# Performance work log

Hardware: AMD Instinct MI355X
Metric: run time of the kernel (lower is better)

## Reference

```python
import jax, jax.numpy as jnp
import numpy as np

DIM = 256          # model dim
H = 8              # num heads
E = DIM // H       # head dim = 32
M = 32             # ball size
NB = 8192          # number of balls
N = NB * M         # total points = 262144
D3 = 3             # spatial dimensionality


def setup_inputs() -> dict:
    key = jax.random.key(0)
    ks = jax.random.split(key, 10)
    s = 1.0 / np.sqrt(DIM)
    return {
        "x": jax.random.normal(ks[0], (N, DIM), jnp.float32),
        "pos": jax.random.normal(ks[1], (N, D3), jnp.float32),
        "w_qkv": jax.random.normal(ks[2], (DIM, 3 * DIM), jnp.float32) * s,
        "b_qkv": jnp.zeros((3 * DIM,), jnp.float32),
        "w_pe": jax.random.normal(ks[3], (D3, DIM), jnp.float32) * (1.0 / np.sqrt(D3)),
        "b_pe": jnp.zeros((DIM,), jnp.float32),
        "w_proj": jax.random.normal(ks[4], (DIM, DIM), jnp.float32) * s,
        "b_proj": jnp.zeros((DIM,), jnp.float32),
        "sigma_att": -1.0 + 0.01 * jax.random.normal(ks[5], (1, H, 1, 1), jnp.float32),
    }


def reference(x, pos, w_qkv, b_qkv, w_pe, b_pe, w_proj, b_proj, sigma_att):
    n = x.shape[0] // M
    pos_b = pos.reshape(n, M, D3)                       # (n, m, 3)

    # eq. 9: relative position embedding wrt ball center
    centers = pos_b.mean(axis=1, keepdims=True)         # (n, 1, 3)
    rel = (pos_b - centers).reshape(n * M, D3)
    x = x + rel @ w_pe + b_pe                           # (N, DIM)

    # qkv projection; layout '(H E K)' with K fastest
    qkv = (x @ w_qkv + b_qkv).reshape(n, M, H, E, 3)
    q = jnp.transpose(qkv[..., 0], (0, 2, 1, 3))        # (n, H, m, E)
    k = jnp.transpose(qkv[..., 1], (0, 2, 1, 3))
    v = jnp.transpose(qkv[..., 2], (0, 2, 1, 3))

    # eq. 10: distance-based attention bias
    diff = pos_b[:, :, None, :] - pos_b[:, None, :, :]  # (n, m, m, 3)
    d2 = jnp.sum(diff * diff, axis=-1)
    dist = jnp.sqrt(jnp.maximum(d2, 1e-12))             # safe sqrt (grad at 0)
    bias = sigma_att * dist[:, None, :, :]              # (n, H, m, m)

    scale = 1.0 / np.sqrt(E)
    scores = jnp.einsum('nhme,nhke->nhmk', q, k) * scale + bias
    attn = jax.nn.softmax(scores, axis=-1)
    out = jnp.einsum('nhmk,nhke->nhme', attn, v)        # (n, H, m, E)
    out = jnp.transpose(out, (0, 2, 1, 3)).reshape(n * M, DIM)
    return out @ w_proj + b_proj
```

## Files before the change

kernel.cpp:

```cpp
#include <hip/hip_runtime.h>

#define NPTS   262144
#define NBALLS 8192
#define MSZ    32

typedef unsigned short u16;
typedef __attribute__((ext_vector_type(8))) unsigned short u16x8;
typedef __attribute__((ext_vector_type(4))) unsigned short u16x4;
typedef __attribute__((ext_vector_type(8))) __bf16 bf16x8;
typedef __attribute__((ext_vector_type(4))) float f32x4;

__device__ inline u16 f2bf(float f) {
    unsigned u = __builtin_bit_cast(unsigned, f);
    u += 0x7fffu + ((u >> 16) & 1u);
    return (u16)(u >> 16);
}

__device__ inline f32x4 mfma16(u16x8 a, u16x8 b, f32x4 c) {
    return __builtin_amdgcn_mfma_f32_16x16x32_bf16(
        __builtin_bit_cast(bf16x8, a), __builtin_bit_cast(bf16x8, b), c, 0, 0, 0);
}

__device__ inline void gload_lds16(const u16* g, u16* l) {
    __builtin_amdgcn_global_load_lds(
        (const __attribute__((address_space(1))) void*)g,
        (__attribute__((address_space(3))) void*)l, 16, 0, 0);
}

__global__ __launch_bounds__(256) void k0_wprep(const float* __restrict__ w_qkv,
                                                const float* __restrict__ b_qkv,
                                                const float* __restrict__ w_proj,
                                                u16* __restrict__ wqkvT,
                                                u16* __restrict__ wpF,
                                                float* __restrict__ bq) {
    int idx = blockIdx.x * 256 + threadIdx.x;
    if (idx < 768 * 256) {
        int cp = idx >> 8, r = idx & 255;
        int k = cp >> 8, rem = cp & 255, h = rem >> 5, e = rem & 31;
        int orig = h * 96 + e * 3 + k;
        wqkvT[cp * 256 + r] = f2bf(w_qkv[r * 768 + orig]);
        if (r == 0) bq[cp] = b_qkv[orig];
    } else {
        int tid2 = idx - 768 * 256;
        int lane = tid2 & 63, ch = tid2 >> 6;
        int hk = ch & 7, gct = ch >> 3;
        int r15 = lane & 15, g4 = lane >> 4;
        u16x8 o;
#pragma unroll
        for (int j = 0; j < 8; ++j)
            o[j] = f2bf(w_proj[(size_t)(hk * 32 + g4 * 8 + j) * 256 + gct * 16 + r15]);
        *(u16x8*)&wpF[(size_t)tid2 * 8] = o;
    }
}

__global__ __launch_bounds__(256) void k0b_xp(const float* __restrict__ x,
                                              const float* __restrict__ pos,
                                              const float* __restrict__ w_pe,
                                              const float* __restrict__ b_pe,
                                              u16* __restrict__ xp) {
    int ball = blockIdx.x, t = threadIdx.x;
    __shared__ float ps[MSZ][3];
    __shared__ float ctr[3];
    if (t < MSZ * 3) ((float*)ps)[t] = pos[(size_t)ball * (MSZ * 3) + t];
    __syncthreads();
    if (t < 3) {
        float s = 0.f;
#pragma unroll
        for (int j = 0; j < MSZ; ++j) s += ps[j][t];
        ctr[t] = s * (1.0f / MSZ);
    }
    __syncthreads();
    int c4 = (t & 63) * 4;
    float4 w0 = *(const float4*)&w_pe[c4];
    float4 w1 = *(const float4*)&w_pe[256 + c4];
    float4 w2 = *(const float4*)&w_pe[512 + c4];
    float4 bp = *(const float4*)&b_pe[c4];
#pragma unroll
    for (int mi = (t >> 6); mi < MSZ; mi += 4) {
        float rx = ps[mi][0] - ctr[0], ry = ps[mi][1] - ctr[1], rz = ps[mi][2] - ctr[2];
        size_t row = (size_t)ball * MSZ + mi;
        float4 xv = *(const float4*)&x[row * 256 + c4];
        u16x4 o;
        o.x = f2bf(xv.x + rx * w0.x + ry * w1.x + rz * w2.x + bp.x);
        o.y = f2bf(xv.y + rx * w0.y + ry * w1.y + rz * w2.y + bp.y);
        o.z = f2bf(xv.z + rx * w0.z + ry * w1.z + rz * w2.z + bp.z);
        o.w = f2bf(xv.w + rx * w0.w + ry * w1.w + rz * w2.w + bp.w);
        *(u16x4*)&xp[row * 256 + c4] = o;
    }
}

__global__ __launch_bounds__(512, 4) void k1_qkv(const u16* __restrict__ xp,
                                                 const u16* __restrict__ wqkvT,
                                                 const float* __restrict__ bq,
                                                 u16* __restrict__ qkv2) {
    __shared__ __align__(16) u16 As[2][128 * 64];
    __shared__ __align__(16) u16 Bs[2][128 * 64];
    int id = blockIdx.x;
    int wk = (id >> 3) + (id & 7) * 1536;
    int ct = wk % 6, rt = wk / 6;
    int t = threadIdx.x;
    int lane = t & 63, wv = t >> 6;
    int r15 = lane & 15, g4 = lane >> 4;
    int wr = wv >> 1, wc = wv & 1;
    int rowbase = rt * 128, colbase = ct * 128;

    f32x4 acc[2][4];
#pragma unroll
    for (int i = 0; i < 2; ++i)
#pragma unroll
        for (int j = 0; j < 4; ++j) acc[i][j] = (f32x4){0.f, 0.f, 0.f, 0.f};

#pragma unroll
    for (int i = 0; i < 2; ++i) {
        int c = i * 512 + t;
        int row = c >> 3, sg = c & 7;
        int gsw = (sg ^ (row & 7)) * 8;
        gload_lds16(&xp[(size_t)(rowbase + row) * 256 + gsw], &As[0][c * 8]);
        gload_lds16(&wqkvT[(size_t)(colbase + row) * 256 + gsw], &Bs[0][c * 8]);
    }
    __syncthreads();

    for (int kt = 0; kt < 4; ++kt) {
        int cur = kt & 1;
        if (kt < 3) {
            int k0 = (kt + 1) * 64;
#pragma unroll
            for (int i = 0; i < 2; ++i) {
                int c = i * 512 + t;
                int row = c >> 3, sg = c & 7;
                int gsw = k0 + (sg ^ (row & 7)) * 8;
                gload_lds16(&xp[(size_t)(rowbase + row) * 256 + gsw], &As[cur ^ 1][c * 8]);
                gload_lds16(&wqkvT[(size_t)(colbase + row) * 256 + gsw], &Bs[cur ^ 1][c * 8]);
            }
        }
#pragma unroll
        for (int ks = 0; ks < 2; ++ks) {
            u16x8 a[2], b[4];
#pragma unroll
            for (int i = 0; i < 2; ++i) {
                int R = wr * 32 + i * 16 + r15;
                a[i] = *(const u16x8*)&As[cur][R * 64 + (((ks * 4 + g4) ^ (R & 7)) * 8)];
            }
#pragma unroll
            for (int j = 0; j < 4; ++j) {
                int C = wc * 64 + j * 16 + r15;
                b[j] = *(const u16x8*)&Bs[cur][C * 64 + (((ks * 4 + g4) ^ (C & 7)) * 8)];
            }
#pragma unroll
            for (int i = 0; i < 2; ++i)
#pragma unroll
                for (int j = 0; j < 4; ++j)
                    acc[i][j] = mfma16(a[i], b[j], acc[i][j]);
        }
        __syncthreads();
    }

    const int ball = rt * 4 + wr;
#pragma unroll
    for (int j = 0; j < 4; ++j) {
        int cp = colbase + wc * 64 + j * 16 + r15;
        float bias = bq[cp];
        int mat = cp >> 8, rem = cp & 255, h = rem >> 5, e = rem & 31;
        size_t base = (size_t)ball * 24576 + mat * 8192 + h * 1024 + e;
#pragma unroll
        for (int i = 0; i < 2; ++i) {
#pragma unroll
            for (int r = 0; r < 4; ++r) {
                int point = i * 16 + g4 * 4 + r;
                qkv2[base + point * 32] = f2bf(acc[i][j][r] + bias);
            }
        }
    }
}

__global__ __launch_bounds__(256) void k23_attnproj(const float* __restrict__ pos,
                                                    const float* __restrict__ sigma,
                                                    const u16* __restrict__ qkv2,
                                                    const u16* __restrict__ wpF,
                                                    const float* __restrict__ bp,
                                                    float* __restrict__ out) {
    int ball = blockIdx.x, t = threadIdx.x;
    __shared__ float ps[MSZ][3];
    __shared__ float dist_s[MSZ][33];
    __shared__ __align__(16) u16 V_s[MSZ][256];
    __shared__ __align__(16) u16 P_s[4][MSZ][40];
    __shared__ __align__(16) u16 ao_s[MSZ][264];

    const size_t ballbase = (size_t)ball * 24576;

    if (t < MSZ * 3) ((float*)ps)[t] = pos[(size_t)ball * (MSZ * 3) + t];
    __syncthreads();
    for (int p = t; p < 1024; p += 256) {
        int m = p >> 5, k = p & 31;
        float dx = ps[m][0] - ps[k][0], dy = ps[m][1] - ps[k][1], dz = ps[m][2] - ps[k][2];
        dist_s[m][k] = sqrtf(fmaxf(dx * dx + dy * dy + dz * dz, 1e-12f));
    }
#pragma unroll
    for (int i = 0; i < 4; ++i) {
        int c = i * 256 + t;
        int h = c >> 7, wi = c & 127;
        int point = wi >> 2, g4w = wi & 3;
        int col8 = h * 32 + g4w * 8;
        int cs = col8 ^ (((point >> 3) & 3) << 4);
        *(u16x8*)&V_s[point][cs] = *(const u16x8*)&qkv2[ballbase + 16384 + (size_t)c * 8];
    }
    __syncthreads();

    int lane = t & 63, wv = t >> 6;
    int r15 = lane & 15, g4 = lane >> 4;
    const float scale = 0.17677669529663687f;

#pragma unroll
    for (int hh = 0; hh < 2; ++hh) {
        int h = wv * 2 + hh;
        float sig = sigma[h];
        u16x8 aq[2], bk[2];
#pragma unroll
        for (int i = 0; i < 2; ++i) {
            aq[i] = *(const u16x8*)&qkv2[ballbase + h * 1024 + (size_t)(i * 16 + r15) * 32 + g4 * 8];
            bk[i] = *(const u16x8*)&qkv2[ballbase + 8192 + h * 1024 + (size_t)(i * 16 + r15) * 32 + g4 * 8];
        }
        f32x4 s[2][2];
#pragma unroll
        for (int i = 0; i < 2; ++i)
#pragma unroll
            for (int j = 0; j < 2; ++j) s[i][j] = (f32x4){0.f, 0.f, 0.f, 0.f};
#pragma unroll
        for (int i = 0; i < 2; ++i)
#pragma unroll
            for (int j = 0; j < 2; ++j)
                s[i][j] = mfma16(aq[i], bk[j], s[i][j]);

#pragma unroll
        for (int i = 0; i < 2; ++i) {
#pragma unroll
            for (int r = 0; r < 4; ++r) {
                int row = i * 16 + g4 * 4 + r;
                float v0 = s[i][0][r] * scale + sig * dist_s[row][r15];
                float v1 = s[i][1][r] * scale + sig * dist_s[row][16 + r15];
                float m = fmaxf(v0, v1);
                m = fmaxf(m, __shfl_xor(m, 1));
                m = fmaxf(m, __shfl_xor(m, 2));
                m = fmaxf(m, __shfl_xor(m, 4));
                m = fmaxf(m, __shfl_xor(m, 8));
                float e0 = __expf(v0 - m), e1 = __expf(v1 - m);
                float su = e0 + e1;
                su += __shfl_xor(su, 1);
                su += __shfl_xor(su, 2);
                su += __shfl_xor(su, 4);
                su += __shfl_xor(su, 8);
                float rin = 1.0f / su;
                P_s[wv][row][r15]      = f2bf(e0 * rin);
                P_s[wv][row][16 + r15] = f2bf(e1 * rin);
            }
        }
        u16x8 pa[2];
#pragma unroll
        for (int i = 0; i < 2; ++i)
            pa[i] = *(const u16x8*)&P_s[wv][i * 16 + r15][g4 * 8];
        u16x8 bv[2];
#pragma unroll
        for (int j = 0; j < 2; ++j) {
#pragma unroll
            for (int jj = 0; jj < 8; ++jj) {
                int kp = g4 * 8 + jj;
                int colv = h * 32 + j * 16 + r15;
                bv[j][jj] = V_s[kp][colv ^ (((kp >> 3) & 3) << 4)];
            }
        }
        f32x4 o[2][2];
#pragma unroll
        for (int i = 0; i < 2; ++i)
#pragma unroll
            for (int j = 0; j < 2; ++j) o[i][j] = (f32x4){0.f, 0.f, 0.f, 0.f};
#pragma unroll
        for (int i = 0; i < 2; ++i)
#pragma unroll
            for (int j = 0; j < 2; ++j)
                o[i][j] = mfma16(pa[i], bv[j], o[i][j]);
#pragma unroll
        for (int i = 0; i < 2; ++i)
#pragma unroll
            for (int j = 0; j < 2; ++j)
#pragma unroll
                for (int r = 0; r < 4; ++r) {
                    int row = i * 16 + g4 * 4 + r;
                    int col = h * 32 + j * 16 + r15;
                    ao_s[row][col] = f2bf(o[i][j][r]);
                }
    }
    __syncthreads();

    f32x4 pacc[4][2];
#pragma unroll
    for (int tt = 0; tt < 4; ++tt)
#pragma unroll
        for (int i = 0; i < 2; ++i) pacc[tt][i] = (f32x4){0.f, 0.f, 0.f, 0.f};
#pragma unroll
    for (int hk = 0; hk < 8; ++hk) {
        u16x8 apj[2];
#pragma unroll
        for (int i = 0; i < 2; ++i)
            apj[i] = *(const u16x8*)&ao_s[i * 16 + r15][hk * 32 + g4 * 8];
#pragma unroll
        for (int tt = 0; tt < 4; ++tt) {
            int gct = wv * 4 + tt;
            u16x8 b = *(const u16x8*)&wpF[(size_t)((gct * 8 + hk) * 64 + lane) * 8];
            pacc[tt][0] = mfma16(apj[0], b, pacc[tt][0]);
            pacc[tt][1] = mfma16(apj[1], b, pacc[tt][1]);
        }
    }
#pragma unroll
    for (int tt = 0; tt < 4; ++tt) {
        int ct = (wv * 4 + tt) * 16;
        float bb = bp[ct + r15];
#pragma unroll
        for (int i = 0; i < 2; ++i)
#pragma unroll
            for (int r = 0; r < 4; ++r) {
                int row = ball * MSZ + i * 16 + g4 * 4 + r;
                out[(size_t)row * 256 + ct + r15] = pacc[tt][i][r] + bb;
            }
    }
}

extern "C" void kernel_launch(void* const* d_in, const int* in_sizes, int n_in,
                              void* d_out, int out_size, void* d_ws, size_t ws_size,
                              hipStream_t stream) {
    (void)in_sizes; (void)n_in; (void)out_size; (void)ws_size;
    const float* x      = (const float*)d_in[0];
    const float* pos    = (const float*)d_in[1];
    const float* w_qkv  = (const float*)d_in[2];
    const float* b_qkv  = (const float*)d_in[3];
    const float* w_pe   = (const float*)d_in[4];
    const float* b_pe   = (const float*)d_in[5];
    const float* w_proj = (const float*)d_in[6];
    const float* b_proj = (const float*)d_in[7];
    const float* sigma  = (const float*)d_in[8];
    float* out = (float*)d_out;

    u16* qkv2   = (u16*)d_ws;
    u16* wqkvT  = qkv2 + (size_t)NPTS * 768;
    u16* wpF    = wqkvT + 768 * 256;
    float* bq   = (float*)(wpF + 65536);
    u16* xp     = (u16*)d_out;

    k0_wprep<<<800, 256, 0, stream>>>(w_qkv, b_qkv, w_proj, wqkvT, wpF, bq);
    k0b_xp<<<NBALLS, 256, 0, stream>>>(x, pos, w_pe, b_pe, xp);
    k1_qkv<<<12288, 512, 0, stream>>>(xp, wqkvT, bq, qkv2);
    k23_attnproj<<<NBALLS, 256, 0, stream>>>(pos, sigma, qkv2, wpF, b_proj, out);
}
```

Before: 482.6 us.

## Fuse positional-embedding add into QKV GEMM A-tile load and vectorize stores

Removes the separate kernel that built a bf16 copy of x plus the relative-position embedding. The QKV GEMM now loads fp32 x into registers, adds the embedding computed from per-ball centers in shared memory, converts to bf16 and writes the swizzled A tile itself, while B is still loaded asynchronously. The MFMA operands are swapped so each lane holds four consecutive output columns, which allows packed 8-byte stores to qkv2 instead of scalar 2-byte stores. The cost is that every one of the six column-tile blocks re-reads fp32 x (twice the bytes of bf16) and redoes the embedding math, and the A loads become synchronous register loads.

```diff
diff --git a/kernel.cpp b/kernel.cpp
--- a/kernel.cpp
+++ b/kernel.cpp
@@ -9,11 +9,16 @@
 typedef __attribute__((ext_vector_type(4))) unsigned short u16x4;
 typedef __attribute__((ext_vector_type(8))) __bf16 bf16x8;
 typedef __attribute__((ext_vector_type(4))) float f32x4;
+typedef __attribute__((ext_vector_type(2))) unsigned u32x2;
 
 __device__ inline u16 f2bf(float f) {
     unsigned u = __builtin_bit_cast(unsigned, f);
     u += 0x7fffu + ((u >> 16) & 1u);
     return (u16)(u >> 16);
+}
+
+__device__ inline unsigned pk2(float lo, float hi) {
+    return (unsigned)f2bf(lo) | ((unsigned)f2bf(hi) << 16);
 }
 
 __device__ inline f32x4 mfma16(u16x8 a, u16x8 b, f32x4 c) {
@@ -53,48 +58,21 @@
     }
 }
 
-__global__ __launch_bounds__(256) void k0b_xp(const float* __restrict__ x,
-                                              const float* __restrict__ pos,
-                                              const float* __restrict__ w_pe,
-                                              const float* __restrict__ b_pe,
-                                              u16* __restrict__ xp) {
-    int ball = blockIdx.x, t = threadIdx.x;
-    __shared__ float ps[MSZ][3];
-    __shared__ float ctr[3];
-    if (t < MSZ * 3) ((float*)ps)[t] = pos[(size_t)ball * (MSZ * 3) + t];
-    __syncthreads();
-    if (t < 3) {
-        float s = 0.f;
-#pragma unroll
-        for (int j = 0; j < MSZ; ++j) s += ps[j][t];
-        ctr[t] = s * (1.0f / MSZ);
-    }
-    __syncthreads();
-    int c4 = (t & 63) * 4;
-    float4 w0 = *(const float4*)&w_pe[c4];
-    float4 w1 = *(const float4*)&w_pe[256 + c4];
-    float4 w2 = *(const float4*)&w_pe[512 + c4];
-    float4 bp = *(const float4*)&b_pe[c4];
-#pragma unroll
-    for (int mi = (t >> 6); mi < MSZ; mi += 4) {
-        float rx = ps[mi][0] - ctr[0], ry = ps[mi][1] - ctr[1], rz = ps[mi][2] - ctr[2];
-        size_t row = (size_t)ball * MSZ + mi;
-        float4 xv = *(const float4*)&x[row * 256 + c4];
-        u16x4 o;
-        o.x = f2bf(xv.x + rx * w0.x + ry * w1.x + rz * w2.x + bp.x);
-        o.y = f2bf(xv.y + rx * w0.y + ry * w1.y + rz * w2.y + bp.y);
-        o.z = f2bf(xv.z + rx * w0.z + ry * w1.z + rz * w2.z + bp.z);
-        o.w = f2bf(xv.w + rx * w0.w + ry * w1.w + rz * w2.w + bp.w);
-        *(u16x4*)&xp[row * 256 + c4] = o;
-    }
-}
-
-__global__ __launch_bounds__(512, 4) void k1_qkv(const u16* __restrict__ xp,
+__global__ __launch_bounds__(512, 4) void k1_qkv(const float* __restrict__ x,
+                                                 const float* __restrict__ pos,
+                                                 const float* __restrict__ w_pe,
+                                                 const float* __restrict__ b_pe,
                                                  const u16* __restrict__ wqkvT,
                                                  const float* __restrict__ bq,
                                                  u16* __restrict__ qkv2) {
     __shared__ __align__(16) u16 As[2][128 * 64];
     __shared__ __align__(16) u16 Bs[2][128 * 64];
+    __shared__ float ps_s[384];
+    __shared__ float ctr_s[4][3];
+    __shared__ float rel_s[128][3];
+    __shared__ float wpe_s[3][256];
+    __shared__ float bpe_s[256];
+
     int id = blockIdx.x;
     int wk = (id >> 3) + (id & 7) * 1536;
     int ct = wk % 6, rt = wk / 6;
@@ -104,33 +82,72 @@
     int wr = wv >> 1, wc = wv & 1;
     int rowbase = rt * 128, colbase = ct * 128;
 
-    f32x4 acc[2][4];
-#pragma unroll
-    for (int i = 0; i < 2; ++i)
-#pragma unroll
-        for (int j = 0; j < 4; ++j) acc[i][j] = (f32x4){0.f, 0.f, 0.f, 0.f};
+    if (t < 384) ps_s[t] = pos[(size_t)rt * 384 + t];
+    if (t < 256) bpe_s[t] = b_pe[t];
+    for (int i = t; i < 768; i += 512) ((float*)wpe_s)[i] = w_pe[i];
+    __syncthreads();
+    if (t < 12) {
+        int b = t / 3, m = t % 3;
+        float s = 0.f;
+#pragma unroll
+        for (int j = 0; j < MSZ; ++j) s += ps_s[(b * 32 + j) * 3 + m];
+        ctr_s[b][m] = s * (1.0f / MSZ);
+    }
+    __syncthreads();
+    if (t < 384) {
+        int p = t / 3, m = t % 3;
+        ((float*)rel_s)[t] = ps_s[t] - ctr_s[p >> 5][m];
+    }
 
 #pragma unroll
     for (int i = 0; i < 2; ++i) {
         int c = i * 512 + t;
         int row = c >> 3, sg = c & 7;
-        int gsw = (sg ^ (row & 7)) * 8;
-        gload_lds16(&xp[(size_t)(rowbase + row) * 256 + gsw], &As[0][c * 8]);
-        gload_lds16(&wqkvT[(size_t)(colbase + row) * 256 + gsw], &Bs[0][c * 8]);
-    }
-    __syncthreads();
+        gload_lds16(&wqkvT[(size_t)(colbase + row) * 256 + (sg ^ (row & 7)) * 8],
+                    &Bs[0][c * 8]);
+    }
+    __syncthreads();
+
+#pragma unroll
+    for (int i = 0; i < 2; ++i) {
+        int c = i * 512 + t;
+        int row = c >> 3, g = c & 7;
+        int k0 = g * 8;
+        float4 xa = *(const float4*)&x[(size_t)(rowbase + row) * 256 + k0];
+        float4 xb = *(const float4*)&x[(size_t)(rowbase + row) * 256 + k0 + 4];
+        float r0 = rel_s[row][0], r1 = rel_s[row][1], r2 = rel_s[row][2];
+        u16x8 o;
+#pragma unroll
+        for (int m = 0; m < 8; ++m) {
+            float xv = (m < 4) ? ((const float*)&xa)[m] : ((const float*)&xb)[m - 4];
+            float v = fmaf(r0, wpe_s[0][k0 + m],
+                      fmaf(r1, wpe_s[1][k0 + m],
+                      fmaf(r2, wpe_s[2][k0 + m], xv))) + bpe_s[k0 + m];
+            o[m] = f2bf(v);
+        }
+        *(u16x8*)&As[0][(row * 8 + (g ^ (row & 7))) * 8] = o;
+    }
+    __syncthreads();
+
+    f32x4 acc[4][2];
+#pragma unroll
+    for (int j = 0; j < 4; ++j)
+#pragma unroll
+        for (int i = 0; i < 2; ++i) acc[j][i] = (f32x4){0.f, 0.f, 0.f, 0.f};
 
     for (int kt = 0; kt < 4; ++kt) {
         int cur = kt & 1;
+        float4 nxa[2], nxb[2];
         if (kt < 3) {
-            int k0 = (kt + 1) * 64;
+            int k0n = (kt + 1) * 64;
 #pragma unroll
             for (int i = 0; i < 2; ++i) {
                 int c = i * 512 + t;
                 int row = c >> 3, sg = c & 7;
-                int gsw = k0 + (sg ^ (row & 7)) * 8;
-                gload_lds16(&xp[(size_t)(rowbase + row) * 256 + gsw], &As[cur ^ 1][c * 8]);
-                gload_lds16(&wqkvT[(size_t)(colbase + row) * 256 + gsw], &Bs[cur ^ 1][c * 8]);
+                gload_lds16(&wqkvT[(size_t)(colbase + row) * 256 + k0n + (sg ^ (row & 7)) * 8],
+                            &Bs[cur ^ 1][c * 8]);
+                nxa[i] = *(const float4*)&x[(size_t)(rowbase + row) * 256 + k0n + sg * 8];
+                nxb[i] = *(const float4*)&x[(size_t)(rowbase + row) * 256 + k0n + sg * 8 + 4];
             }
         }
 #pragma unroll
@@ -147,10 +164,30 @@
                 b[j] = *(const u16x8*)&Bs[cur][C * 64 + (((ks * 4 + g4) ^ (C & 7)) * 8)];
             }
 #pragma unroll
-            for (int i = 0; i < 2; ++i)
-#pragma unroll
-                for (int j = 0; j < 4; ++j)
-                    acc[i][j] = mfma16(a[i], b[j], acc[i][j]);
+            for (int j = 0; j < 4; ++j)
+#pragma unroll
+                for (int i = 0; i < 2; ++i)
+                    acc[j][i] = mfma16(b[j], a[i], acc[j][i]);
+        }
+        if (kt < 3) {
+            int k0n = (kt + 1) * 64;
+#pragma unroll
+            for (int i = 0; i < 2; ++i) {
+                int c = i * 512 + t;
+                int row = c >> 3, g = c & 7;
+                float r0 = rel_s[row][0], r1 = rel_s[row][1], r2 = rel_s[row][2];
+                u16x8 o;
+#pragma unroll
+                for (int m = 0; m < 8; ++m) {
+                    float xv = (m < 4) ? ((const float*)&nxa[i])[m] : ((const float*)&nxb[i])[m - 4];
+                    int kk = k0n + g * 8 + m;
+                    float v = fmaf(r0, wpe_s[0][kk],
+                              fmaf(r1, wpe_s[1][kk],
+                              fmaf(r2, wpe_s[2][kk], xv))) + bpe_s[kk];
+                    o[m] = f2bf(v);
+                }
+                *(u16x8*)&As[cur ^ 1][(row * 8 + (g ^ (row & 7))) * 8] = o;
+            }
         }
         __syncthreads();
     }
@@ -158,17 +195,16 @@
     const int ball = rt * 4 + wr;
 #pragma unroll
     for (int j = 0; j < 4; ++j) {
-        int cp = colbase + wc * 64 + j * 16 + r15;
-        float bias = bq[cp];
-        int mat = cp >> 8, rem = cp & 255, h = rem >> 5, e = rem & 31;
-        size_t base = (size_t)ball * 24576 + mat * 8192 + h * 1024 + e;
+        int cp0 = colbase + wc * 64 + j * 16 + g4 * 4;
+        float4 bias = *(const float4*)&bq[cp0];
+        int mat = cp0 >> 8, rem = cp0 & 255, h = rem >> 5, e0 = rem & 31;
+        size_t base = (size_t)ball * 24576 + mat * 8192 + h * 1024 + e0;
 #pragma unroll
         for (int i = 0; i < 2; ++i) {
-#pragma unroll
-            for (int r = 0; r < 4; ++r) {
-                int point = i * 16 + g4 * 4 + r;
-                qkv2[base + point * 32] = f2bf(acc[i][j][r] + bias);
-            }
+            int point = i * 16 + r15;
+            unsigned lo = pk2(acc[j][i][0] + bias.x, acc[j][i][1] + bias.y);
+            unsigned hi = pk2(acc[j][i][2] + bias.z, acc[j][i][3] + bias.w);
+            *(u32x2*)&qkv2[base + point * 32] = (u32x2){lo, hi};
         }
     }
 }
@@ -343,10 +379,8 @@
     u16* wqkvT  = qkv2 + (size_t)NPTS * 768;
     u16* wpF    = wqkvT + 768 * 256;
     float* bq   = (float*)(wpF + 65536);
-    u16* xp     = (u16*)d_out;
 
     k0_wprep<<<800, 256, 0, stream>>>(w_qkv, b_qkv, w_proj, wqkvT, wpF, bq);
-    k0b_xp<<<NBALLS, 256, 0, stream>>>(x, pos, w_pe, b_pe, xp);
-    k1_qkv<<<12288, 512, 0, stream>>>(xp, wqkvT, bq, qkv2);
+    k1_qkv<<<12288, 512, 0, stream>>>(x, pos, w_pe, b_pe, wqkvT, bq, qkv2);
     k23_attnproj<<<NBALLS, 256, 0, stream>>>(pos, sigma, qkv2, wpF, b_proj, out);
 }
```

Result: no change. 475.3 us (-1.5%).
